# Performance work log

Hardware: AMD Instinct MI355X
Metric: run time of the kernel (lower is better)

## Reference

```python
import jax, jax.numpy as jnp
import numpy as np

TAU = 0.1
LAM = 1.0
THRESHOLD = 32  # undefined global in source; set to L//2
B, D, L = 4096, 4096, 64


def setup_inputs() -> dict:
    key = jax.random.key(0)
    k1, k2, k3 = jax.random.split(key, 3)
    return {
        "x_pred_batch": jax.random.normal(k1, (B, D), dtype=jnp.float32),
        "y_pred_batch": jax.random.normal(k2, (B, D), dtype=jnp.float32),
        "label_batch": jax.random.randint(k3, (B, L), 0, 2, dtype=jnp.int32),
    }


def reference(x_pred_batch, y_pred_batch, label_batch):
    # l2-normalize each embedding once; cosine sims become plain dots
    xn = x_pred_batch / jnp.linalg.norm(x_pred_batch, axis=-1, keepdims=True)
    yn = y_pred_batch / jnp.linalg.norm(y_pred_batch, axis=-1, keepdims=True)

    # positive error: mean_i exp((1 - cos(x_i, y_i)) / tau)
    cos_pos = jnp.sum(xn * yn, axis=-1)  # [B]
    pos_error = jnp.mean(jnp.exp((1.0 - cos_pos) / TAU))

    # negatives: samples with more than THRESHOLD zero labels
    zero_counts = jnp.sum(label_batch == 0, axis=-1)  # [B]
    neg_mask = zero_counts > THRESHOLD                # [B] bool
    # pairs (i in neg, j not in neg)
    pair_mask = neg_mask[:, None] & (~neg_mask)[None, :]  # [B, B]
    cnt = jnp.sum(pair_mask)  # n_neg * n_nonneg (loop counter in source)

    def neg_error(zn):
        sim = zn @ zn.T  # [B, B] pairwise cosine sims
        s = jnp.sum(jnp.exp(sim / TAU) * pair_mask)
        return jnp.where(cnt > 0, s / jnp.maximum(cnt, 1).astype(zn.dtype), 0.0)

    return pos_error + LAM * (neg_error(xn) + neg_error(yn))
```

## Files before the change

kernel.cpp:

```cpp
#include <hip/hip_runtime.h>

#define B_SZ 4096
#define D_SZ 4096
#define L_SZ 64
#define TAU_INV 10.0f
#define THRESH 32
#define NT 32
#define TRI (NT * (NT + 1) / 2)

#define DB4 2048

#define FP4_PRESCALE 160.0f
#define EXP_SCALE4 (TAU_INV / 25600.0f)

typedef __attribute__((ext_vector_type(8))) short bf16x8;
typedef __attribute__((ext_vector_type(4))) float f32x4;
typedef __attribute__((ext_vector_type(8))) int i32x8;

union fragu { i32x8 v; int4 h[2]; };

__device__ __forceinline__ unsigned short f2bf(float f) {
    union { float f; unsigned u; } v; v.f = f;
    unsigned r = v.u + 0x7fffu + ((v.u >> 16) & 1u);
    return (unsigned short)(r >> 16);
}

__device__ __forceinline__ unsigned f2fp4(float f) {
    float a = fabsf(f);
    unsigned code = (unsigned)(a >= 0.25f) + (a >= 0.75f) + (a >= 1.25f) + (a >= 1.75f)
                  + (a >= 2.5f) + (a >= 3.5f) + (a >= 5.0f);
    return code | ((__float_as_uint(f) >> 28) & 8u);
}

__device__ __forceinline__ unsigned short enc4(float4 v, float s) {
    unsigned n0 = f2fp4(v.x * s), n1 = f2fp4(v.y * s),
             n2 = f2fp4(v.z * s), n3 = f2fp4(v.w * s);
    return (unsigned short)(n0 | (n1 << 4) | (n2 << 8) | (n3 << 12));
}

__device__ __forceinline__ void gload_lds16(const void* g, void* l) {
    __builtin_amdgcn_global_load_lds(
        (const __attribute__((address_space(1))) void*)g,
        (__attribute__((address_space(3))) void*)l, 16, 0, 0);
}

__global__ void init_kernel(double* acc, int* n_neg) {
    int t = threadIdx.x;
    if (t < 35) acc[t] = 0.0;
    if (t == 0) *n_neg = 0;
}

__global__ void mask_kernel(const int* __restrict__ labels, int* __restrict__ neg_mask,
                            int* __restrict__ n_neg) {
    int row = blockIdx.x * blockDim.x + threadIdx.x;
    if (row >= B_SZ) return;
    const int4* lr = reinterpret_cast<const int4*>(labels + (size_t)row * L_SZ);
    int cnt = 0;
#pragma unroll
    for (int i = 0; i < L_SZ / 4; i++) {
        int4 v = lr[i];
        cnt += (v.x == 0) + (v.y == 0) + (v.z == 0) + (v.w == 0);
    }
    int neg = (cnt > THRESH) ? 1 : 0;
    neg_mask[row] = neg;
    if (neg) atomicAdd(n_neg, 1);
}

__global__ __launch_bounds__(256) void norm_prep_fp4_kernel(const float* __restrict__ X,
                                                            const float* __restrict__ Y,
                                                            unsigned char* __restrict__ Xq,
                                                            unsigned char* __restrict__ Yq,
                                                            double* __restrict__ acc) {
    int row = blockIdx.x;
    int t = threadIdx.x;
    int lane = t & 63;
    int w = t >> 6;
    const float4* xr = reinterpret_cast<const float4*>(X + (size_t)row * D_SZ);
    const float4* yr = reinterpret_cast<const float4*>(Y + (size_t)row * D_SZ);
    float4 xv[4], yv[4];
    float sx = 0.f, sy = 0.f, dxy = 0.f;
#pragma unroll
    for (int i = 0; i < 4; i++) {
        xv[i] = xr[t + 256 * i];
        yv[i] = yr[t + 256 * i];
        sx  += xv[i].x * xv[i].x + xv[i].y * xv[i].y + xv[i].z * xv[i].z + xv[i].w * xv[i].w;
        sy  += yv[i].x * yv[i].x + yv[i].y * yv[i].y + yv[i].z * yv[i].z + yv[i].w * yv[i].w;
        dxy += xv[i].x * yv[i].x + xv[i].y * yv[i].y + xv[i].z * yv[i].z + xv[i].w * yv[i].w;
    }
#pragma unroll
    for (int off = 32; off > 0; off >>= 1) {
        sx  += __shfl_xor(sx, off, 64);
        sy  += __shfl_xor(sy, off, 64);
        dxy += __shfl_xor(dxy, off, 64);
    }
    __shared__ float wred[4][3];
    if (lane == 0) { wred[w][0] = sx; wred[w][1] = sy; wred[w][2] = dxy; }
    __syncthreads();
    float tsx  = wred[0][0] + wred[1][0] + wred[2][0] + wred[3][0];
    float tsy  = wred[0][1] + wred[1][1] + wred[2][1] + wred[3][1];
    float tdxy = wred[0][2] + wred[1][2] + wred[2][2] + wred[3][2];
    float inx = 1.0f / sqrtf(tsx);
    float iny = 1.0f / sqrtf(tsy);
    if (t == 0) {
        float cosv = tdxy * inx * iny;
        atomicAdd(&acc[3 + (row & 31)], (double)expf((1.0f - cosv) * TAU_INV));
    }
    float ex = inx * FP4_PRESCALE;
    float ey = iny * FP4_PRESCALE;
    unsigned short* xd = reinterpret_cast<unsigned short*>(Xq) + (size_t)row * 1024;
    unsigned short* yd = reinterpret_cast<unsigned short*>(Yq) + (size_t)row * 1024;
#pragma unroll
    for (int i = 0; i < 4; i++) {
        xd[256 * i + t] = enc4(xv[i], ex);
        yd[256 * i + t] = enc4(yv[i], ey);
    }
}

__global__ __launch_bounds__(256) void norm_kernel(const float* __restrict__ X,
                                                   const float* __restrict__ Y,
                                                   float* __restrict__ inv_nx,
                                                   float* __restrict__ inv_ny,
                                                   double* __restrict__ pos_sum) {
    int row = blockIdx.x;
    int t = threadIdx.x;
    const float4* xr = reinterpret_cast<const float4*>(X + (size_t)row * D_SZ);
    const float4* yr = reinterpret_cast<const float4*>(Y + (size_t)row * D_SZ);
    float sx = 0.f, sy = 0.f, dxy = 0.f;
    for (int i = t; i < D_SZ / 4; i += 256) {
        float4 xvv = xr[i];
        float4 yvv = yr[i];
        sx  += xvv.x * xvv.x + xvv.y * xvv.y + xvv.z * xvv.z + xvv.w * xvv.w;
        sy  += yvv.x * yvv.x + yvv.y * yvv.y + yvv.z * yvv.z + yvv.w * yvv.w;
        dxy += xvv.x * yvv.x + xvv.y * yvv.y + xvv.z * yvv.z + xvv.w * yvv.w;
    }
    __shared__ float rs0[256], rs1[256], rs2[256];
    rs0[t] = sx; rs1[t] = sy; rs2[t] = dxy;
    __syncthreads();
    for (int off = 128; off > 0; off >>= 1) {
        if (t < off) { rs0[t] += rs0[t + off]; rs1[t] += rs1[t + off]; rs2[t] += rs2[t + off]; }
        __syncthreads();
    }
    if (t == 0) {
        float inx = 1.0f / sqrtf(rs0[0]);
        float iny = 1.0f / sqrtf(rs1[0]);
        inv_nx[row] = inx;
        inv_ny[row] = iny;
        float cosv = rs2[0] * inx * iny;
        atomicAdd(pos_sum, (double)expf((1.0f - cosv) * TAU_INV));
    }
}

__global__ __launch_bounds__(256, 3) void sim_fused_fp4_kernel(const unsigned char* __restrict__ Xq,
                                                               const unsigned char* __restrict__ Yq,
                                                               const int* __restrict__ neg_mask,
                                                               double* __restrict__ accum2) {
    int b = blockIdx.x;
    int wg = (b & 7) * 132 + (b >> 3);
    int mat = (wg >= TRI) ? 1 : 0;
    int u = wg - mat * TRI;
    int ti = 0;
    while (u >= NT - ti) { u -= NT - ti; ti++; }
    int tj = ti + u;
    const unsigned char* Zq = mat ? Yq : Xq;

    __shared__ __align__(16) unsigned char As[128 * 128];
    __shared__ __align__(16) unsigned char Bs[128 * 128];

    int t = threadIdx.x;
    int lane = t & 63;
    int w = t >> 6;
    int wr = w >> 1, wc = w & 1;
    int gi0 = ti * 128, gj0 = tj * 128;

    f32x4 acc[4][4];
#pragma unroll
    for (int m = 0; m < 4; m++)
#pragma unroll
        for (int n = 0; n < 4; n++) acc[m][n] = (f32x4){0.f, 0.f, 0.f, 0.f};

    int srow_l = lane >> 3;
    int psx = (lane & 7) ^ srow_l;
    int scol_sw = (((psx & 3) << 1) | (psx >> 2)) * 16;

    int lrow = lane & 15;
    int qh = lane >> 4;
    int rsw = lrow & 7;
    int off0 = (qh ^ rsw) * 16;
    int off1 = ((qh + 4) ^ rsw) * 16;

    for (int kb = 0; kb < DB4; kb += 128) {
        if (kb) __syncthreads();
#pragma unroll
        for (int c = 0; c < 4; c++) {
            int s = w * 4 + c;
            int r = s * 8 + srow_l;
            gload_lds16(&Zq[(size_t)(gi0 + r) * DB4 + kb + scol_sw], &As[s * 1024]);
            gload_lds16(&Zq[(size_t)(gj0 + r) * DB4 + kb + scol_sw], &Bs[s * 1024]);
        }
        __syncthreads();

#pragma unroll
        for (int hs = 0; hs < 2; hs++) {
            int lo = hs ? off1 : off0;
            int hi = hs ? off0 : off1;

            fragu bfr[4];
#pragma unroll
            for (int n = 0; n < 4; n++) {
                int base = (wc * 64 + n * 16 + lrow) * 128;
                bfr[n].h[0] = *reinterpret_cast<const int4*>(&Bs[base + lo]);
                bfr[n].h[1] = *reinterpret_cast<const int4*>(&Bs[base + hi]);
            }
            fragu afr[4];
#pragma unroll
            for (int m = 0; m < 4; m++) {
                int base = (wr * 64 + m * 16 + lrow) * 128;
                afr[m].h[0] = *reinterpret_cast<const int4*>(&As[base + lo]);
                afr[m].h[1] = *reinterpret_cast<const int4*>(&As[base + hi]);
            }
#pragma unroll
            for (int m = 0; m < 4; m++)
#pragma unroll
                for (int n = 0; n < 4; n++)
                    acc[m][n] = __builtin_amdgcn_mfma_scale_f32_16x16x128_f8f6f4(
                        afr[m].v, bfr[n].v, acc[m][n], 4, 4,
                        0, 0x7F7F7F7F, 0, 0x7F7F7F7F);
        }
    }

    int lr4 = (lane >> 4) * 4;
    int lc = lane & 15;
    int negr[4][4], negc[4];
#pragma unroll
    for (int n = 0; n < 4; n++) negc[n] = neg_mask[gj0 + wc * 64 + n * 16 + lc];
#pragma unroll
    for (int m = 0; m < 4; m++)
#pragma unroll
        for (int j = 0; j < 4; j++) negr[m][j] = neg_mask[gi0 + wr * 64 + m * 16 + lr4 + j];

    float s = 0.f;
#pragma unroll
    for (int m = 0; m < 4; m++) {
#pragma unroll
        for (int n = 0; n < 4; n++) {
            int gj = gj0 + wc * 64 + n * 16 + lc;
            f32x4 a = acc[m][n];
#pragma unroll
            for (int j = 0; j < 4; j++) {
                int gi = gi0 + wr * 64 + m * 16 + lr4 + j;
                if (gi < gj && (negr[m][j] != negc[n]))
                    s += expf(a[j] * EXP_SCALE4);
            }
        }
    }

    float* red = reinterpret_cast<float*>(As);
    __syncthreads();
    red[t] = s;
    __syncthreads();
    for (int off = 128; off > 0; off >>= 1) {
        if (t < off) red[t] += red[t + off];
        __syncthreads();
    }
    if (t == 0) atomicAdd(&accum2[mat], (double)red[0]);
}

#define BMF 128
#define BKF 32
#define LDKF 40
__global__ __launch_bounds__(256) void sim_mfma_kernel(const float* __restrict__ Z,
                                                       const float* __restrict__ inv_n,
                                                       const int* __restrict__ neg_mask,
                                                       double* __restrict__ accum) {
    int ti = blockIdx.y, tj = blockIdx.x;
    if (ti > tj) return;

    __shared__ unsigned short As[BMF][LDKF];
    __shared__ unsigned short Bs[BMF][LDKF];

    int t = threadIdx.x;
    int lane = t & 63;
    int w = t >> 6;
    int wr = w >> 1, wc = w & 1;
    int gi0 = ti * BMF, gj0 = tj * BMF;

    f32x4 acc[4][4];
#pragma unroll
    for (int m = 0; m < 4; m++)
#pragma unroll
        for (int n = 0; n < 4; n++) acc[m][n] = (f32x4){0.f, 0.f, 0.f, 0.f};

    int srow = t >> 3;
    int scol = (t & 7) * 4;

    float invA[4], invB[4];
#pragma unroll
    for (int i = 0; i < 4; i++) {
        invA[i] = inv_n[gi0 + srow + i * 32];
        invB[i] = inv_n[gj0 + srow + i * 32];
    }

    int lrow = lane & 15;
    int ko = (lane >> 4) * 8;

    for (int k0 = 0; k0 < D_SZ; k0 += BKF) {
        __syncthreads();
#pragma unroll
        for (int i = 0; i < 4; i++) {
            int r = srow + i * 32;
            float4 av = *reinterpret_cast<const float4*>(&Z[(size_t)(gi0 + r) * D_SZ + k0 + scol]);
            float4 bv = *reinterpret_cast<const float4*>(&Z[(size_t)(gj0 + r) * D_SZ + k0 + scol]);
            ushort4 ap, bp;
            ap.x = f2bf(av.x * invA[i]); ap.y = f2bf(av.y * invA[i]);
            ap.z = f2bf(av.z * invA[i]); ap.w = f2bf(av.w * invA[i]);
            bp.x = f2bf(bv.x * invB[i]); bp.y = f2bf(bv.y * invB[i]);
            bp.z = f2bf(bv.z * invB[i]); bp.w = f2bf(bv.w * invB[i]);
            *reinterpret_cast<ushort4*>(&As[r][scol]) = ap;
            *reinterpret_cast<ushort4*>(&Bs[r][scol]) = bp;
        }
        __syncthreads();

        bf16x8 afr[4], bfr[4];
#pragma unroll
        for (int m = 0; m < 4; m++)
            afr[m] = *reinterpret_cast<const bf16x8*>(&As[wr * 64 + m * 16 + lrow][ko]);
#pragma unroll
        for (int n = 0; n < 4; n++)
            bfr[n] = *reinterpret_cast<const bf16x8*>(&Bs[wc * 64 + n * 16 + lrow][ko]);
#pragma unroll
        for (int m = 0; m < 4; m++)
#pragma unroll
            for (int n = 0; n < 4; n++)
                acc[m][n] = __builtin_amdgcn_mfma_f32_16x16x32_bf16(afr[m], bfr[n], acc[m][n], 0, 0, 0);
    }

    int lr4 = (lane >> 4) * 4;
    int lc = lane & 15;
    int negr[4][4], negc[4];
#pragma unroll
    for (int n = 0; n < 4; n++) negc[n] = neg_mask[gj0 + wc * 64 + n * 16 + lc];
#pragma unroll
    for (int m = 0; m < 4; m++)
#pragma unroll
        for (int j = 0; j < 4; j++) negr[m][j] = neg_mask[gi0 + wr * 64 + m * 16 + lr4 + j];

    float s = 0.f;
#pragma unroll
    for (int m = 0; m < 4; m++) {
#pragma unroll
        for (int n = 0; n < 4; n++) {
            int gj = gj0 + wc * 64 + n * 16 + lc;
            f32x4 a = acc[m][n];
#pragma unroll
            for (int j = 0; j < 4; j++) {
                int gi = gi0 + wr * 64 + m * 16 + lr4 + j;
                if (gi < gj && (negr[m][j] != negc[n]))
                    s += expf(a[j] * TAU_INV);
            }
        }
    }

    __shared__ float red[256];
    red[t] = s;
    __syncthreads();
    for (int off = 128; off > 0; off >>= 1) {
        if (t < off) red[t] += red[t + off];
        __syncthreads();
    }
    if (t == 0) atomicAdd(accum, (double)red[0]);
}

__global__ void final_kernel(const double* __restrict__ acc, const int* __restrict__ n_neg,
                             float* __restrict__ out) {
    double pos = acc[0];
    for (int i = 3; i < 35; i++) pos += acc[i];
    pos /= (double)B_SZ;
    long long nn = *n_neg;
    long long cnt = nn * ((long long)B_SZ - nn);
    double neg = (cnt > 0) ? (acc[1] + acc[2]) / (double)cnt : 0.0;
    out[0] = (float)(pos + neg);
}

extern "C" void kernel_launch(void* const* d_in, const int* in_sizes, int n_in,
                              void* d_out, int out_size, void* d_ws, size_t ws_size,
                              hipStream_t stream) {
    const float* X = (const float*)d_in[0];
    const float* Y = (const float*)d_in[1];
    const int* labels = (const int*)d_in[2];
    float* out = (float*)d_out;

    char* ws = (char*)d_ws;
    double* acc = (double*)ws;
    int* n_neg = (int*)(ws + 512);
    int* neg_mask = (int*)(ws + 1024);
    float* inv_nx = (float*)(ws + 20480);
    float* inv_ny = (float*)(ws + 36864);

    const size_t FP4_BYTES = (size_t)B_SZ * DB4;
    const size_t HDR = 65536;

    init_kernel<<<1, 64, 0, stream>>>(acc, n_neg);
    mask_kernel<<<B_SZ / 256, 256, 0, stream>>>(labels, neg_mask, n_neg);

    if (ws_size >= HDR + 2 * FP4_BYTES) {
        unsigned char* Xq = (unsigned char*)(ws + HDR);
        unsigned char* Yq = (unsigned char*)(ws + HDR + FP4_BYTES);
        norm_prep_fp4_kernel<<<B_SZ, 256, 0, stream>>>(X, Y, Xq, Yq, acc);
        sim_fused_fp4_kernel<<<2 * TRI, 256, 0, stream>>>(Xq, Yq, neg_mask, &acc[1]);
    } else {
        dim3 grid(NT, NT);
        norm_kernel<<<B_SZ, 256, 0, stream>>>(X, Y, inv_nx, inv_ny, &acc[0]);
        sim_mfma_kernel<<<grid, 256, 0, stream>>>(X, inv_nx, neg_mask, &acc[1]);
        sim_mfma_kernel<<<grid, 256, 0, stream>>>(Y, inv_ny, neg_mask, &acc[2]);
    }

    final_kernel<<<1, 1, 0, stream>>>(acc, n_neg, out);
}
```

Baseline: 105.4 us.

## Repack FP4 operands so each MFMA fragment needs one 16-byte LDS read

The prep kernel now packs eight consecutive values into each 32-bit word, and each thread loads two adjacent float4s instead of strided ones. The GEMM inner loop reads a single 16-byte chunk per fragment and copies it into both halves of the operand register, where it previously made two LDS reads. This relies on the FP4 MFMA variant reading only the low 128 bits of each operand, and on A and B sharing the same k permutation so the dot products are unchanged. The goal is to halve LDS fragment traffic in the GEMM loop; the added risk is correctness if the operand-width assumption or the k-ordering consistency is wrong.

Result: no change. 104.2 us (median of 2 runs) (-1.1%).

```diff
diff --git a/kernel.cpp b/kernel.cpp
--- a/kernel.cpp
+++ b/kernel.cpp
@@ -32,10 +32,11 @@
     return code | ((__float_as_uint(f) >> 28) & 8u);
 }
 
-__device__ __forceinline__ unsigned short enc4(float4 v, float s) {
-    unsigned n0 = f2fp4(v.x * s), n1 = f2fp4(v.y * s),
-             n2 = f2fp4(v.z * s), n3 = f2fp4(v.w * s);
-    return (unsigned short)(n0 | (n1 << 4) | (n2 << 8) | (n3 << 12));
+__device__ __forceinline__ unsigned enc8(float4 a, float4 b, float s) {
+    return  f2fp4(a.x * s)        | (f2fp4(a.y * s) << 4)
+         | (f2fp4(a.z * s) << 8)  | (f2fp4(a.w * s) << 12)
+         | (f2fp4(b.x * s) << 16) | (f2fp4(b.y * s) << 20)
+         | (f2fp4(b.z * s) << 24) | (f2fp4(b.w * s) << 28);
 }
 
 __device__ __forceinline__ void gload_lds16(const void* g, void* l) {
@@ -80,12 +81,17 @@
     float4 xv[4], yv[4];
     float sx = 0.f, sy = 0.f, dxy = 0.f;
 #pragma unroll
-    for (int i = 0; i < 4; i++) {
-        xv[i] = xr[t + 256 * i];
-        yv[i] = yr[t + 256 * i];
-        sx  += xv[i].x * xv[i].x + xv[i].y * xv[i].y + xv[i].z * xv[i].z + xv[i].w * xv[i].w;
-        sy  += yv[i].x * yv[i].x + yv[i].y * yv[i].y + yv[i].z * yv[i].z + yv[i].w * yv[i].w;
-        dxy += xv[i].x * yv[i].x + xv[i].y * yv[i].y + xv[i].z * yv[i].z + xv[i].w * yv[i].w;
+    for (int j = 0; j < 2; j++) {
+#pragma unroll
+        for (int q = 0; q < 2; q++) {
+            float4 xvv = xr[512 * j + 2 * t + q];
+            float4 yvv = yr[512 * j + 2 * t + q];
+            xv[2 * j + q] = xvv;
+            yv[2 * j + q] = yvv;
+            sx  += xvv.x * xvv.x + xvv.y * xvv.y + xvv.z * xvv.z + xvv.w * xvv.w;
+            sy  += yvv.x * yvv.x + yvv.y * yvv.y + yvv.z * yvv.z + yvv.w * yvv.w;
+            dxy += xvv.x * yvv.x + xvv.y * yvv.y + xvv.z * yvv.z + xvv.w * yvv.w;
+        }
     }
 #pragma unroll
     for (int off = 32; off > 0; off >>= 1) {
@@ -107,12 +113,12 @@
     }
     float ex = inx * FP4_PRESCALE;
     float ey = iny * FP4_PRESCALE;
-    unsigned short* xd = reinterpret_cast<unsigned short*>(Xq) + (size_t)row * 1024;
-    unsigned short* yd = reinterpret_cast<unsigned short*>(Yq) + (size_t)row * 1024;
-#pragma unroll
-    for (int i = 0; i < 4; i++) {
-        xd[256 * i + t] = enc4(xv[i], ex);
-        yd[256 * i + t] = enc4(yv[i], ey);
+    unsigned* xd = reinterpret_cast<unsigned*>(Xq + (size_t)row * DB4);
+    unsigned* yd = reinterpret_cast<unsigned*>(Yq + (size_t)row * DB4);
+#pragma unroll
+    for (int j = 0; j < 2; j++) {
+        xd[256 * j + t] = enc8(xv[2 * j], xv[2 * j + 1], ex);
+        yd[256 * j + t] = enc8(yv[2 * j], yv[2 * j + 1], ey);
     }
 }
 
@@ -201,22 +207,21 @@
 
 #pragma unroll
         for (int hs = 0; hs < 2; hs++) {
-            int lo = hs ? off1 : off0;
-            int hi = hs ? off0 : off1;
+            int off = hs ? off1 : off0;
 
             fragu bfr[4];
 #pragma unroll
             for (int n = 0; n < 4; n++) {
-                int base = (wc * 64 + n * 16 + lrow) * 128;
-                bfr[n].h[0] = *reinterpret_cast<const int4*>(&Bs[base + lo]);
-                bfr[n].h[1] = *reinterpret_cast<const int4*>(&Bs[base + hi]);
+                int4 xb = *reinterpret_cast<const int4*>(&Bs[(wc * 64 + n * 16 + lrow) * 128 + off]);
+                bfr[n].h[0] = xb;
+                bfr[n].h[1] = xb;
             }
             fragu afr[4];
 #pragma unroll
             for (int m = 0; m < 4; m++) {
-                int base = (wr * 64 + m * 16 + lrow) * 128;
-                afr[m].h[0] = *reinterpret_cast<const int4*>(&As[base + lo]);
-                afr[m].h[1] = *reinterpret_cast<const int4*>(&As[base + hi]);
+                int4 xa = *reinterpret_cast<const int4*>(&As[(wr * 64 + m * 16 + lrow) * 128 + off]);
+                afr[m].h[0] = xa;
+                afr[m].h[1] = xa;
             }
 #pragma unroll
             for (int m = 0; m < 4; m++)
```
